# Kernel tuning notes

Hardware: AMD Instinct MI355X
Metric: run time of the kernel (lower is better)

## Reference

```python
import jax, jax.numpy as jnp
import numpy as np

K_F = 3
NUM = K_F * K_F - 1          # 8 non-center neighbors
IDX_REF = NUM // 2           # 4 (center insertion index)
PROP_TIME = 18
AFFINITY_GAMMA = 0.5
B, H, W = 4, 480, 640


def _bilinear(img, y, x):
    """Bilinear sample img [H,W] at float coords y,x [K,H,W]; zero outside."""
    Hh, Ww = img.shape
    y0 = jnp.floor(y)
    x0 = jnp.floor(x)

    def gather(yy, xx):
        valid = (yy >= 0) & (yy < Hh) & (xx >= 0) & (xx < Ww)
        yi = jnp.clip(yy.astype(jnp.int32), 0, Hh - 1)
        xi = jnp.clip(xx.astype(jnp.int32), 0, Ww - 1)
        return jnp.where(valid, img[yi, xi], 0.0)

    wy = y - y0
    wx = x - x0
    return ((1 - wy) * (1 - wx) * gather(y0, x0)
            + (1 - wy) * wx * gather(y0, x0 + 1)
            + wy * (1 - wx) * gather(y0 + 1, x0)
            + wy * wx * gather(y0 + 1, x0 + 1))


def _deform_prop(feat, dy, dx, aff):
    """Modulated deformable 3x3 conv with all-ones weight, zero bias, ch=1.
    feat [B,1,H,W]; dy,dx,aff [B,9,H,W]. Output = sum_k aff_k * sample_k."""
    b, _, h, w = feat.shape
    ky = jnp.array([-1, -1, -1, 0, 0, 0, 1, 1, 1], feat.dtype)
    kx = jnp.array([-1, 0, 1, -1, 0, 1, -1, 0, 1], feat.dtype)
    gy = jnp.arange(h, dtype=feat.dtype)[:, None]   # [H,1]
    gx = jnp.arange(w, dtype=feat.dtype)[None, :]   # [1,W]
    py = gy[None, None] + ky[None, :, None, None] + dy  # [B,9,H,W]
    px = gx[None, None] + kx[None, :, None, None] + dx
    samp = jax.vmap(_bilinear)(feat[:, 0], py, px)      # [B,9,H,W]
    return jnp.sum(samp * aff, axis=1, keepdims=True)


def _affinity_normalization(aff, scale):
    # TGASS: tanh / (gamma*num), abs-sum normalize (clamped at 1), reference = 1 - sum
    aff = jnp.tanh(aff) / (scale + 1e-8)
    s = jnp.sum(jnp.abs(aff), axis=1, keepdims=True) + 1e-4
    s = jnp.maximum(s, 1.0)
    aff = aff / s
    aff_ref = 1.0 - jnp.sum(aff, axis=1, keepdims=True)
    return jnp.concatenate([aff[:, :IDX_REF], aff_ref, aff[:, IDX_REF:]], axis=1)


def setup_inputs() -> dict:
    key = jax.random.key(0)
    k1, k2, k3, k4, k5 = jax.random.split(key, 5)
    feat_init = jax.random.uniform(k1, (B, 1, H, W), jnp.float32) * 10.0
    guidance = jax.random.normal(k2, (B, 24, H, W), jnp.float32)
    confidence = jax.random.uniform(k3, (B, 1, H, W), jnp.float32)
    dense = jax.random.uniform(k4, (B, 1, H, W), jnp.float32) * 10.0
    mask = (jax.random.uniform(k5, (B, 1, H, W)) < 0.05).astype(jnp.float32)
    feat_fix = dense * mask
    aff_scale_const = jnp.full((1,), AFFINITY_GAMMA * NUM, jnp.float32)
    return {"feat_init": feat_init, "guidance": guidance,
            "confidence": confidence, "feat_fix": feat_fix,
            "aff_scale_const": aff_scale_const}


def reference(feat_init, guidance, confidence, feat_fix, aff_scale_const):
    b = feat_init.shape[0]
    h, w = feat_init.shape[2], feat_init.shape[3]
    # offsets: chunk guidance into (o1, o2, aff), interleave, insert zero at center
    o1, o2, aff_g = jnp.split(guidance, 3, axis=1)
    off = jnp.concatenate([o1, o2], axis=1).reshape(b, NUM, 2, h, w)
    zc = jnp.zeros((b, 1, 2, h, w), off.dtype)
    off = jnp.concatenate([off[:, :IDX_REF], zc, off[:, IDX_REF:]], axis=1)
    dy, dx = off[:, :, 0], off[:, :, 1]          # [B,9,H,W]
    aff = _affinity_normalization(aff_g, aff_scale_const)

    # preserve_input: fixed-pixel mask (ch_f == 1)
    mask_fix = (feat_fix > 0.0).astype(feat_init.dtype)
    conf = (1.0 - mask_fix) * confidence + mask_fix
    feat = (1.0 - mask_fix) * feat_init + mask_fix * feat_fix

    def step(f, _):
        f = _deform_prop(f * conf, dy, dx, aff)
        f = (1.0 - mask_fix) * f + mask_fix * feat_fix
        return f, None

    feat, _ = jax.lax.scan(step, feat, None, length=PROP_TIME)
    return feat
```

## Files before the change

kernel.cpp:

```cpp
#include <hip/hip_runtime.h>
#include <hip/hip_fp16.h>


#define HH 480
#define WW 640
#define BB 4
#define HWSZ (HH * WW)
#define NPIX (BB * HWSZ)
#define PROP_T 18
#define SLACK 704

struct f2u { float x, y; };

__device__ __forceinline__ float fast_tanh(float x) {
    x = fminf(fmaxf(x, -15.0f), 15.0f);
    float e = __expf(2.0f * x);
    return __fdividef(e - 1.0f, e + 1.0f);
}

__global__ __launch_bounds__(256) void precompute_kernel(
    const float* __restrict__ feat_init,
    const float* __restrict__ guid,
    const float* __restrict__ confidence,
    const float* __restrict__ feat_fix,
    const float* __restrict__ aff_scale,
    float* __restrict__ g0,
    float2* __restrict__ ac_mid,
    float2* __restrict__ ac_last,
    int* __restrict__ idxArr,
    uint2* __restrict__ wArr) {
    const int x = blockIdx.x * 64 + threadIdx.x;
    const int y = blockIdx.y * 4 + threadIdx.y;
    const int b = blockIdx.z;
    const int q = y * WW + x;
    const int pix = b * HWSZ + q;
    const float* gb = guid + (size_t)b * 24 * HWSZ + q;

    {
        float ff = feat_fix[pix];
        float m  = (ff > 0.0f) ? 1.0f : 0.0f;
        float km = 1.0f - m;
        float conf = km * confidence[pix] + m;
        float f0   = km * feat_init[pix] + m * ff;
        g0[pix] = f0 * conf;
        ac_mid[pix]  = make_float2(conf * km, conf * m * ff);
        ac_last[pix] = make_float2(km, m * ff);
    }

    const float inv_scale = __fdividef(1.0f, aff_scale[0] + 1e-8f);
    float t[8];
    float ssum = 1e-4f;
#pragma unroll
    for (int j = 0; j < 8; ++j) {
        float v = fast_tanh(gb[(16 + j) * HWSZ]) * inv_scale;
        t[j] = v;
        ssum += fabsf(v);
    }
    ssum = fmaxf(ssum, 1.0f);
    float rs = __fdividef(1.0f, ssum);
    float asum = 0.0f;
#pragma unroll
    for (int j = 0; j < 8; ++j) { t[j] *= rs; asum += t[j]; }
    const float aref = 1.0f - asum;

    const float yf = (float)y, xf = (float)x;
    constexpr int KY[9] = {-1, -1, -1, 0, 0, 0, 1, 1, 1};
    constexpr int KX[9] = {-1, 0, 1, -1, 0, 1, -1, 0, 1};
#pragma unroll
    for (int k = 0; k < 9; ++k) {
        float dy, dx, ak;
        if (k == 4) {
            dy = 0.0f; dx = 0.0f; ak = aref;
        } else {
            const int n = (k < 4) ? k : (k - 1);
            dy = gb[(2 * n) * HWSZ];
            dx = gb[(2 * n + 1) * HWSZ];
            ak = t[n];
        }
        float py = yf + (float)KY[k] + dy;
        float px = xf + (float)KX[k] + dx;
        float y0f = floorf(py), x0f = floorf(px);
        float wy = py - y0f, wx = px - x0f;
        int y0 = (int)y0f, x0 = (int)x0f;
        float vy0 = (y0 >= 0 && y0 < HH) ? 1.0f : 0.0f;
        float vy1 = (y0 >= -1 && y0 < HH - 1) ? 1.0f : 0.0f;
        float vx0 = (x0 >= 0 && x0 < WW) ? 1.0f : 0.0f;
        float vx1 = (x0 >= -1 && x0 < WW - 1) ? 1.0f : 0.0f;
        float omwy = 1.0f - wy, omwx = 1.0f - wx;
        float w00 = omwy * omwx * vy0 * vx0 * ak;
        float w01 = omwy * wx  * vy0 * vx1 * ak;
        float w10 = wy * omwx  * vy1 * vx0 * ak;
        float w11 = wy * wx    * vy1 * vx1 * ak;
        int yc = min(max(y0, -1), HH - 1);
        int xc = min(max(x0, -1), WW - 1);
        int idx = b * HWSZ + yc * WW + xc;

        idxArr[k * NPIX + pix] = idx;
        __half2 hab = __floats2half2_rn(w00, w01);
        __half2 hcd = __floats2half2_rn(w10, w11);
        uint2 wr;
        wr.x = *reinterpret_cast<unsigned int*>(&hab);
        wr.y = *reinterpret_cast<unsigned int*>(&hcd);
        wArr[k * NPIX + pix] = wr;
    }
}

__global__ __launch_bounds__(256) void step_kernel(
    const float* __restrict__ fin,
    float* __restrict__ fout,
    const int* __restrict__ idxArr,
    const uint2* __restrict__ wArr,
    const float2* __restrict__ ac) {
    const int pix = blockIdx.x * 256 + threadIdx.x;
    float acc = 0.0f;
#pragma unroll
    for (int k = 0; k < 9; ++k) {
        int idx = idxArr[k * NPIX + pix];
        uint2 wr = wArr[k * NPIX + pix];
        const float* p = fin + idx;
        f2u r0 = *reinterpret_cast<const f2u*>(p);
        f2u r1 = *reinterpret_cast<const f2u*>(p + WW);
        float2 wab = __half22float2(*reinterpret_cast<__half2*>(&wr.x));
        float2 wcd = __half22float2(*reinterpret_cast<__half2*>(&wr.y));
        acc += wab.x * r0.x + wab.y * r0.y + wcd.x * r1.x + wcd.y * r1.y;
    }
    float2 c2 = ac[pix];
    fout[pix] = c2.x * acc + c2.y;
}

extern "C" void kernel_launch(void* const* d_in, const int* in_sizes, int n_in,
                              void* d_out, int out_size, void* d_ws, size_t ws_size,
                              hipStream_t stream) {
    const float* feat_init  = (const float*)d_in[0];
    const float* guidance   = (const float*)d_in[1];
    const float* confidence = (const float*)d_in[2];
    const float* feat_fix   = (const float*)d_in[3];
    const float* aff_scale  = (const float*)d_in[4];

    const size_t bufFloats = (size_t)NPIX + 2 * SLACK;
    float* bufA = (float*)d_ws;
    float* bufB = bufA + bufFloats;
    float2* acMid  = (float2*)(bufB + bufFloats);
    float2* acLast = acMid + NPIX;
    int*   idxArr  = (int*)(acLast + NPIX);
    uint2* wArr    = (uint2*)(idxArr + 9 * (size_t)NPIX);
    float* fA = bufA + SLACK;
    float* fB = bufB + SLACK;

    hipMemsetAsync(bufA, 0, bufFloats * sizeof(float), stream);
    hipMemsetAsync(bufB, 0, bufFloats * sizeof(float), stream);

    {
        dim3 blk(64, 4, 1);
        dim3 grd(WW / 64, HH / 4, BB);
        precompute_kernel<<<grd, blk, 0, stream>>>(
            feat_init, guidance, confidence, feat_fix, aff_scale,
            fA, acMid, acLast, idxArr, wArr);
    }

    for (int t = 0; t < PROP_T; ++t) {
        const float* fin = (t & 1) ? fB : fA;
        float* fout = (t == PROP_T - 1) ? (float*)d_out : ((t & 1) ? fA : fB);
        const float2* ac = (t == PROP_T - 1) ? acLast : acMid;
        step_kernel<<<NPIX / 256, 256, 0, stream>>>(fin, fout, idxArr, wArr, ac);
    }
}
```

Before: 766.7 us.

## Fuse propagation into persistent cooperative kernel with register-resident sampling descriptors

Replaces the precompute kernel plus 18 step launches with one cooperative persistent kernel. Each thread keeps its pixels' gather indices and packed bilinear weights in registers across all iterations and separates steps with grid.sync. Weights are compressed to an fp16 affinity plus 8-bit fractional wy/wx, and the center tap is handled directly. Border handling is folded into the descriptor, and only the slack regions are memset. This cuts the per-step descriptor traffic and launch overhead, at the cost of grid-wide barriers, heavy register pressure, and reduced weight precision, which may change accuracy.

```diff
diff --git a/kernel.cpp b/kernel.cpp
--- a/kernel.cpp
+++ b/kernel.cpp
@@ -1,5 +1,8 @@
 #include <hip/hip_runtime.h>
 #include <hip/hip_fp16.h>
+#include <hip/hip_cooperative_groups.h>
+
+namespace cg = cooperative_groups;
 
 
 #define HH 480
@@ -9,6 +12,7 @@
 #define NPIX (BB * HWSZ)
 #define PROP_T 18
 #define SLACK 704
+#define NTHR 256
 
 struct f2u { float x, y; };
 
@@ -18,114 +22,193 @@
     return __fdividef(e - 1.0f, e + 1.0f);
 }
 
-__global__ __launch_bounds__(256) void precompute_kernel(
+__device__ __forceinline__ float affinities(const float* gb, float inv_scale,
+                                            float t[8]) {
+    float ssum = 1e-4f;
+#pragma unroll
+    for (int j = 0; j < 8; ++j) {
+        float v = fast_tanh(gb[(16 + j) * HWSZ]) * inv_scale;
+        t[j] = v; ssum += fabsf(v);
+    }
+    ssum = fmaxf(ssum, 1.0f);
+    float rs = __fdividef(1.0f, ssum);
+    float asum = 0.0f;
+#pragma unroll
+    for (int j = 0; j < 8; ++j) { t[j] *= rs; asum += t[j]; }
+    return 1.0f - asum;
+}
+
+__device__ __forceinline__ void make_desc(int b, int y, int x, int k,
+                                          float dy, float dx, float ak,
+                                          int& idx_out, unsigned& w_out) {
+    float py = (float)(y + k / 3 - 1) + dy;
+    float px = (float)(x + k % 3 - 1) + dx;
+    float y0f = floorf(py), x0f = floorf(px);
+    float wy = py - y0f, wx = px - x0f;
+    int y0 = (int)y0f, x0 = (int)x0f;
+    if (y0 == -1)                 { ak *= wy;        wy = 1.0f; }
+    else if (y0 == HH - 1)        { ak *= 1.0f - wy; wy = 0.0f; }
+    else if (y0 < -1 || y0 >= HH) { ak = 0.0f; }
+    if (x0 == -1)                 { ak *= wx;        wx = 1.0f; }
+    else if (x0 == WW - 1)        { ak *= 1.0f - wx; wx = 0.0f; }
+    else if (x0 < -1 || x0 >= WW) { ak = 0.0f; }
+    int yc = min(max(y0, -1), HH - 1);
+    int xc = min(max(x0, -1), WW - 1);
+    idx_out = b * HWSZ + yc * WW + xc;
+    unsigned uy = (unsigned)(int)(wy * 255.0f + 0.5f);
+    unsigned ux = (unsigned)(int)(wx * 255.0f + 0.5f);
+    w_out = ((unsigned)__half_as_ushort(__float2half(ak)) << 16)
+          | (uy << 8) | ux;
+}
+
+__device__ __forceinline__ float sample_acc(const float* __restrict__ fin,
+                                            int idx, unsigned u, float acc) {
+    float ak = __half2float(__ushort_as_half((unsigned short)(u >> 16)));
+    float wy = (float)((u >> 8) & 0xffu) * (1.0f / 255.0f);
+    float wx = (float)(u & 0xffu) * (1.0f / 255.0f);
+    const float* p = fin + idx;
+    f2u r0 = *reinterpret_cast<const f2u*>(p);
+    f2u r1 = *reinterpret_cast<const f2u*>(p + WW);
+    float bot = ak * wy;
+    float top = ak - bot;
+    float omwx = 1.0f - wx;
+    acc = fmaf(top * omwx, r0.x, acc);
+    acc = fmaf(top * wx,   r0.y, acc);
+    acc = fmaf(bot * omwx, r1.x, acc);
+    acc = fmaf(bot * wx,   r1.y, acc);
+    return acc;
+}
+
+template <int PXT, int MINW>
+__global__ __launch_bounds__(NTHR, MINW) void persist_kernel(
+    const float* __restrict__ feat_init,
+    const float* __restrict__ guid,
+    const float* __restrict__ confidence,
+    const float* __restrict__ feat_fix,
+    const float* __restrict__ aff_scale,
+    float* __restrict__ fA,
+    float* __restrict__ fB,
+    float* __restrict__ out)
+{
+    cg::grid_group grid = cg::this_grid();
+    const int base = blockIdx.x * (NTHR * PXT) + threadIdx.x;
+
+    int      idxd[PXT][8];
+    unsigned wpk[PXT][8];
+    unsigned pxc[PXT];
+    float    ffp[PXT];
+
+    const float inv_scale = __fdividef(1.0f, aff_scale[0] + 1e-8f);
+
+#pragma unroll
+    for (int i = 0; i < PXT; ++i) {
+        const int pix = base + i * NTHR;
+        const int b = pix / HWSZ;
+        const int q = pix - b * HWSZ;
+        const int y = q / WW;
+        const int x = q - y * WW;
+        const float* gb = guid + (size_t)b * 24 * HWSZ + q;
+
+        float ff = feat_fix[pix];
+        float m  = (ff > 0.0f) ? 1.0f : 0.0f;
+        float km = 1.0f - m;
+        float conf = km * confidence[pix] + m;
+        float f0   = km * feat_init[pix] + m * ff;
+        fA[pix] = f0 * conf;
+        ffp[i] = m * ff;
+
+        float t[8];
+        float aref = affinities(gb, inv_scale, t);
+        pxc[i] = ((unsigned)__half_as_ushort(__float2half(aref)) << 16)
+               | (unsigned)__half_as_ushort(__float2half(conf));
+
+#pragma unroll
+        for (int n = 0; n < 8; ++n) {
+            const int k = (n < 4) ? n : (n + 1);
+            float dy = gb[(2 * n) * HWSZ];
+            float dx = gb[(2 * n + 1) * HWSZ];
+            make_desc(b, y, x, k, dy, dx, t[n], idxd[i][n], wpk[i][n]);
+        }
+    }
+
+#pragma unroll 1
+    for (int t = 0; t < PROP_T; ++t) {
+        grid.sync();
+        const float* fin = (t & 1) ? fB : fA;
+        float* fout = (t == PROP_T - 1) ? out : ((t & 1) ? fA : fB);
+#pragma unroll
+        for (int i = 0; i < PXT; ++i) {
+            const int pix = base + i * NTHR;
+            unsigned pc = pxc[i];
+            float aref = __half2float(__ushort_as_half((unsigned short)(pc >> 16)));
+            float conf = __half2float(__ushort_as_half((unsigned short)(pc & 0xffffu)));
+            float acc = aref * fin[pix];
+#pragma unroll
+            for (int n = 0; n < 8; ++n)
+                acc = sample_acc(fin, idxd[i][n], wpk[i][n], acc);
+            float km = (ffp[i] > 0.0f) ? 0.0f : 1.0f;
+            float fnew = fmaf(km, acc, ffp[i]);
+            fout[pix] = (t == PROP_T - 1) ? fnew : conf * fnew;
+        }
+    }
+}
+
+__global__ __launch_bounds__(NTHR) void precompute_kernel(
     const float* __restrict__ feat_init,
     const float* __restrict__ guid,
     const float* __restrict__ confidence,
     const float* __restrict__ feat_fix,
     const float* __restrict__ aff_scale,
     float* __restrict__ g0,
-    float2* __restrict__ ac_mid,
-    float2* __restrict__ ac_last,
+    float4* __restrict__ ac_mid,
+    float4* __restrict__ ac_last,
     int* __restrict__ idxArr,
-    uint2* __restrict__ wArr) {
-    const int x = blockIdx.x * 64 + threadIdx.x;
-    const int y = blockIdx.y * 4 + threadIdx.y;
-    const int b = blockIdx.z;
-    const int q = y * WW + x;
-    const int pix = b * HWSZ + q;
+    unsigned* __restrict__ wArr) {
+    const int pix = blockIdx.x * NTHR + threadIdx.x;
+    const int b = pix / HWSZ;
+    const int q = pix - b * HWSZ;
+    const int y = q / WW;
+    const int x = q - y * WW;
     const float* gb = guid + (size_t)b * 24 * HWSZ + q;
 
-    {
-        float ff = feat_fix[pix];
-        float m  = (ff > 0.0f) ? 1.0f : 0.0f;
-        float km = 1.0f - m;
-        float conf = km * confidence[pix] + m;
-        float f0   = km * feat_init[pix] + m * ff;
-        g0[pix] = f0 * conf;
-        ac_mid[pix]  = make_float2(conf * km, conf * m * ff);
-        ac_last[pix] = make_float2(km, m * ff);
-    }
+    float ff = feat_fix[pix];
+    float m  = (ff > 0.0f) ? 1.0f : 0.0f;
+    float km = 1.0f - m;
+    float conf = km * confidence[pix] + m;
+    float f0   = km * feat_init[pix] + m * ff;
+    g0[pix] = f0 * conf;
 
     const float inv_scale = __fdividef(1.0f, aff_scale[0] + 1e-8f);
     float t[8];
-    float ssum = 1e-4f;
-#pragma unroll
-    for (int j = 0; j < 8; ++j) {
-        float v = fast_tanh(gb[(16 + j) * HWSZ]) * inv_scale;
-        t[j] = v;
-        ssum += fabsf(v);
-    }
-    ssum = fmaxf(ssum, 1.0f);
-    float rs = __fdividef(1.0f, ssum);
-    float asum = 0.0f;
-#pragma unroll
-    for (int j = 0; j < 8; ++j) { t[j] *= rs; asum += t[j]; }
-    const float aref = 1.0f - asum;
-
-    const float yf = (float)y, xf = (float)x;
-    constexpr int KY[9] = {-1, -1, -1, 0, 0, 0, 1, 1, 1};
-    constexpr int KX[9] = {-1, 0, 1, -1, 0, 1, -1, 0, 1};
-#pragma unroll
-    for (int k = 0; k < 9; ++k) {
-        float dy, dx, ak;
-        if (k == 4) {
-            dy = 0.0f; dx = 0.0f; ak = aref;
-        } else {
-            const int n = (k < 4) ? k : (k - 1);
-            dy = gb[(2 * n) * HWSZ];
-            dx = gb[(2 * n + 1) * HWSZ];
-            ak = t[n];
-        }
-        float py = yf + (float)KY[k] + dy;
-        float px = xf + (float)KX[k] + dx;
-        float y0f = floorf(py), x0f = floorf(px);
-        float wy = py - y0f, wx = px - x0f;
-        int y0 = (int)y0f, x0 = (int)x0f;
-        float vy0 = (y0 >= 0 && y0 < HH) ? 1.0f : 0.0f;
-        float vy1 = (y0 >= -1 && y0 < HH - 1) ? 1.0f : 0.0f;
-        float vx0 = (x0 >= 0 && x0 < WW) ? 1.0f : 0.0f;
-        float vx1 = (x0 >= -1 && x0 < WW - 1) ? 1.0f : 0.0f;
-        float omwy = 1.0f - wy, omwx = 1.0f - wx;
-        float w00 = omwy * omwx * vy0 * vx0 * ak;
-        float w01 = omwy * wx  * vy0 * vx1 * ak;
-        float w10 = wy * omwx  * vy1 * vx0 * ak;
-        float w11 = wy * wx    * vy1 * vx1 * ak;
-        int yc = min(max(y0, -1), HH - 1);
-        int xc = min(max(x0, -1), WW - 1);
-        int idx = b * HWSZ + yc * WW + xc;
-
-        idxArr[k * NPIX + pix] = idx;
-        __half2 hab = __floats2half2_rn(w00, w01);
-        __half2 hcd = __floats2half2_rn(w10, w11);
-        uint2 wr;
-        wr.x = *reinterpret_cast<unsigned int*>(&hab);
-        wr.y = *reinterpret_cast<unsigned int*>(&hcd);
-        wArr[k * NPIX + pix] = wr;
-    }
-}
-
-__global__ __launch_bounds__(256) void step_kernel(
+    float aref = affinities(gb, inv_scale, t);
+    ac_mid[pix]  = make_float4(conf * km, conf * m * ff, aref, 0.0f);
+    ac_last[pix] = make_float4(km, m * ff, aref, 0.0f);
+
+#pragma unroll
+    for (int n = 0; n < 8; ++n) {
+        const int k = (n < 4) ? n : (n + 1);
+        float dy = gb[(2 * n) * HWSZ];
+        float dx = gb[(2 * n + 1) * HWSZ];
+        int idx; unsigned w;
+        make_desc(b, y, x, k, dy, dx, t[n], idx, w);
+        idxArr[n * NPIX + pix] = idx;
+        wArr[n * NPIX + pix] = w;
+    }
+}
+
+__global__ __launch_bounds__(NTHR) void step_kernel(
     const float* __restrict__ fin,
     float* __restrict__ fout,
     const int* __restrict__ idxArr,
-    const uint2* __restrict__ wArr,
-    const float2* __restrict__ ac) {
-    const int pix = blockIdx.x * 256 + threadIdx.x;
-    float acc = 0.0f;
-#pragma unroll
-    for (int k = 0; k < 9; ++k) {
-        int idx = idxArr[k * NPIX + pix];
-        uint2 wr = wArr[k * NPIX + pix];
-        const float* p = fin + idx;
-        f2u r0 = *reinterpret_cast<const f2u*>(p);
-        f2u r1 = *reinterpret_cast<const f2u*>(p + WW);
-        float2 wab = __half22float2(*reinterpret_cast<__half2*>(&wr.x));
-        float2 wcd = __half22float2(*reinterpret_cast<__half2*>(&wr.y));
-        acc += wab.x * r0.x + wab.y * r0.y + wcd.x * r1.x + wcd.y * r1.y;
-    }
-    float2 c2 = ac[pix];
-    fout[pix] = c2.x * acc + c2.y;
+    const unsigned* __restrict__ wArr,
+    const float4* __restrict__ ac) {
+    const int pix = blockIdx.x * NTHR + threadIdx.x;
+    float4 c = ac[pix];
+    float acc = c.z * fin[pix];
+#pragma unroll
+    for (int n = 0; n < 8; ++n)
+        acc = sample_acc(fin, idxArr[n * NPIX + pix], wArr[n * NPIX + pix], acc);
+    fout[pix] = fmaf(c.x, acc, c.y);
 }
 
 extern "C" void kernel_launch(void* const* d_in, const int* in_sizes, int n_in,
@@ -140,28 +223,62 @@
     const size_t bufFloats = (size_t)NPIX + 2 * SLACK;
     float* bufA = (float*)d_ws;
     float* bufB = bufA + bufFloats;
-    float2* acMid  = (float2*)(bufB + bufFloats);
-    float2* acLast = acMid + NPIX;
-    int*   idxArr  = (int*)(acLast + NPIX);
-    uint2* wArr    = (uint2*)(idxArr + 9 * (size_t)NPIX);
+    float4* acMid  = (float4*)(bufB + bufFloats);
+    float4* acLast = acMid + NPIX;
+    int*      idxArr = (int*)(acLast + NPIX);
+    unsigned* wArr   = (unsigned*)(idxArr + 8 * (size_t)NPIX);
     float* fA = bufA + SLACK;
     float* fB = bufB + SLACK;
-
-    hipMemsetAsync(bufA, 0, bufFloats * sizeof(float), stream);
-    hipMemsetAsync(bufB, 0, bufFloats * sizeof(float), stream);
+    float* outp = (float*)d_out;
+
+    hipMemsetAsync(bufA, 0, SLACK * sizeof(float), stream);
+    hipMemsetAsync(bufA + SLACK + NPIX, 0, SLACK * sizeof(float), stream);
+    hipMemsetAsync(bufB, 0, SLACK * sizeof(float), stream);
+    hipMemsetAsync(bufB + SLACK + NPIX, 0, SLACK * sizeof(float), stream);
+
+    void* args[] = {
+        (void*)&feat_init, (void*)&guidance, (void*)&confidence,
+        (void*)&feat_fix, (void*)&aff_scale,
+        (void*)&fA, (void*)&fB, (void*)&outp
+    };
+
+    int dev = 0;
+    hipGetDevice(&dev);
+    int cu = 0;
+    hipDeviceGetAttribute(&cu, hipDeviceAttributeMultiprocessorCount, dev);
+    if (cu <= 0) cu = 256;
 
     {
-        dim3 blk(64, 4, 1);
-        dim3 grd(WW / 64, HH / 4, BB);
-        precompute_kernel<<<grd, blk, 0, stream>>>(
-            feat_init, guidance, confidence, feat_fix, aff_scale,
-            fA, acMid, acLast, idxArr, wArr);
-    }
-
+        const int nblk = NPIX / (NTHR * 10);
+        int occ = 0;
+        hipError_t qe = hipOccupancyMaxActiveBlocksPerMultiprocessor(
+            &occ, reinterpret_cast<const void*>(&persist_kernel<10, 2>), NTHR, 0);
+        if (qe == hipSuccess && occ * cu >= nblk) {
+            hipError_t le = hipLaunchCooperativeKernel(
+                reinterpret_cast<void*>(&persist_kernel<10, 2>),
+                dim3(nblk), dim3(NTHR), args, 0, stream);
+            if (le == hipSuccess) return;
+        }
+    }
+    {
+        const int nblk = NPIX / (NTHR * 20);
+        int occ = 0;
+        hipError_t qe = hipOccupancyMaxActiveBlocksPerMultiprocessor(
+            &occ, reinterpret_cast<const void*>(&persist_kernel<20, 1>), NTHR, 0);
+        if (qe == hipSuccess && occ * cu >= nblk) {
+            hipError_t le = hipLaunchCooperativeKernel(
+                reinterpret_cast<void*>(&persist_kernel<20, 1>),
+                dim3(nblk), dim3(NTHR), args, 0, stream);
+            if (le == hipSuccess) return;
+        }
+    }
+    precompute_kernel<<<NPIX / NTHR, NTHR, 0, stream>>>(
+        feat_init, guidance, confidence, feat_fix, aff_scale,
+        fA, acMid, acLast, idxArr, wArr);
     for (int t = 0; t < PROP_T; ++t) {
         const float* fin = (t & 1) ? fB : fA;
-        float* fout = (t == PROP_T - 1) ? (float*)d_out : ((t & 1) ? fA : fB);
-        const float2* ac = (t == PROP_T - 1) ? acLast : acMid;
-        step_kernel<<<NPIX / 256, 256, 0, stream>>>(fin, fout, idxArr, wArr, ac);
-    }
-}
+        float* fout = (t == PROP_T - 1) ? outp : ((t & 1) ? fA : fB);
+        const float4* ac = (t == PROP_T - 1) ? acLast : acMid;
+        step_kernel<<<NPIX / NTHR, NTHR, 0, stream>>>(fin, fout, idxArr, wArr, ac);
+    }
+}
```

Measured after the change: 1.334 ms. 73.9% more time.
